# Optimization experiments

Hardware: AMD Instinct MI355X
Metric: run time of the kernel (lower is better)

Reference implementation:

```python
import jax, jax.numpy as jnp
import numpy as np

T, N, E, F, H, OUT = 6, 50000, 800000, 32, 64, 16


def _glorot(key, shape):
    lim = np.sqrt(6.0 / (shape[0] + shape[1])).astype(np.float32)
    return jax.random.uniform(key, shape, jnp.float32, -lim, lim)


def setup_inputs() -> dict:
    key = jax.random.key(0)
    ks = jax.random.split(key, 12)
    return {
        "xs": jax.random.normal(ks[0], (T, N, F), jnp.float32),
        "edge_index": jax.random.randint(ks[1], (T, 2, E), 0, N, jnp.int32),
        # GCNConv weights/biases for the z, r, h gates
        "Wz": _glorot(ks[2], (F, H)), "bz": jnp.zeros((H,), jnp.float32),
        "Wr": _glorot(ks[3], (F, H)), "br": jnp.zeros((H,), jnp.float32),
        "Wh": _glorot(ks[4], (F, H)), "bh": jnp.zeros((H,), jnp.float32),
        # Linear(2H -> H) per gate
        "Lz_W": _glorot(ks[5], (2 * H, H)), "Lz_b": jnp.zeros((H,), jnp.float32),
        "Lr_W": _glorot(ks[6], (2 * H, H)), "Lr_b": jnp.zeros((H,), jnp.float32),
        "Lh_W": _glorot(ks[7], (2 * H, H)), "Lh_b": jnp.zeros((H,), jnp.float32),
        # final Linear(H -> 16)
        "out_W": _glorot(ks[8], (H, OUT)), "out_b": jnp.zeros((OUT,), jnp.float32),
    }


def _gcn(x, W, b, src, dst):
    """GCNConv: D^-1/2 (A+I) D^-1/2 X W + b, edge list form."""
    n = x.shape[0]
    xw = x @ W  # [N,H] project first (cheaper than per-edge)
    loop = jnp.arange(n, dtype=src.dtype)
    s = jnp.concatenate([src, loop])
    d = jnp.concatenate([dst, loop])
    deg = jax.ops.segment_sum(jnp.ones_like(d, jnp.float32), d, num_segments=n)
    dinv = jnp.where(deg > 0, jax.lax.rsqrt(deg), 0.0)
    norm = dinv[s] * dinv[d]          # [E+N]
    msg = xw[s] * norm[:, None]       # gather + scale
    agg = jax.ops.segment_sum(msg, d, num_segments=n)  # scatter-add
    return agg + b


def reference(xs, edge_index, Wz, bz, Wr, br, Wh, bh,
              Lz_W, Lz_b, Lr_W, Lr_b, Lh_W, Lh_b, out_W, out_b):
    n = xs.shape[1]

    def step(h, inp):
        x, src, dst = inp
        Z = jax.nn.sigmoid(jnp.concatenate([_gcn(x, Wz, bz, src, dst), h], -1) @ Lz_W + Lz_b)
        R = jax.nn.sigmoid(jnp.concatenate([_gcn(x, Wr, br, src, dst), h], -1) @ Lr_W + Lr_b)
        Ht = jnp.tanh(jnp.concatenate([_gcn(x, Wh, bh, src, dst), h * R], -1) @ Lh_W + Lh_b)
        h_new = Z * h + (1.0 - Z) * Ht
        return h_new, None

    h0 = jnp.zeros((n, Wz.shape[1]), xs.dtype)
    h_final, _ = jax.lax.scan(step, h0, (xs, edge_index[:, 0], edge_index[:, 1]))
    return h_final @ out_W + out_b  # [N,16]
```

## Files before the change

### kernel.cpp

```cpp
#include <hip/hip_runtime.h>
#include <hip/hip_bf16.h>

#define TT 6
#define NN 50000
#define EE 800000
#define FF 32
#define HH 64
#define OO 16

#define NB 256
#define DPB 196
#define CHUNK 4096
#define CAP 4096

#define WFRAG_N 19456

typedef unsigned short ushort_t;
typedef unsigned char uchar_t;
typedef short short8 __attribute__((ext_vector_type(8)));
typedef float f32x4 __attribute__((ext_vector_type(4)));

__device__ __forceinline__ float ubf(ushort_t v){ return __uint_as_float(((unsigned)v) << 16); }
__device__ __forceinline__ ushort_t f2b(float f){
  unsigned u = __float_as_uint(f);
  return (ushort_t)((u + 0x7FFFu + ((u >> 16) & 1u)) >> 16);
}
__device__ __forceinline__ float lo16f(unsigned u){ return __uint_as_float(u << 16); }
__device__ __forceinline__ float hi16f(unsigned u){ return __uint_as_float(u & 0xFFFF0000u); }

__global__ void prepall_kernel(const float* __restrict__ Wz,const float* __restrict__ bz,
                               const float* __restrict__ Wr,const float* __restrict__ br,
                               const float* __restrict__ Wh,const float* __restrict__ bh,
                               const float* __restrict__ Lz,const float* __restrict__ Lzb,
                               const float* __restrict__ Lr,const float* __restrict__ Lrb,
                               const float* __restrict__ Lh,const float* __restrict__ Lhb,
                               const float* __restrict__ oW,const float* __restrict__ ob,
                               short* __restrict__ wfrag, float* __restrict__ wbias,
                               int* __restrict__ bcur){
  int bid = blockIdx.x, tid = threadIdx.x;
  if (bid < 76){
    int idx = bid*256 + tid;
    int slot = idx >> 9, lane = (idx >> 3) & 63, j = idx & 7;
    int q = lane >> 4, l15 = lane & 15;
    float val;
    if (slot < 36){
      int g, kc, ncol;
      if (slot < 24){ int nt = slot/3; kc = slot - nt*3; ncol = nt*16 + l15;
                      g = (ncol < 64) ? 0 : 1; ncol &= 63; }
      else          { int s2 = slot-24; int nt = s2/3; kc = s2 - nt*3;
                      ncol = nt*16 + l15; g = 2; }
      const float* W = (g==0)?Wz:((g==1)?Wr:Wh);
      const float* L = (g==0)?Lz:((g==1)?Lr:Lh);
      int k = kc*32 + q*8 + j;
      if (k < 32){
        float s = 0.f;
        for (int m = 0; m < 64; m++) s += W[k*64+m] * L[m*64+ncol];
        val = s;
      } else val = L[(32+k)*64 + ncol];
    } else {
      int kc = slot - 36;
      int k = kc*32 + q*8 + j;
      val = oW[k*16 + l15];
    }
    wfrag[idx] = (short)f2b(val);
  } else {
    if (tid < 192){
      int g = tid >> 6, j = tid & 63;
      const float* L  = (g==0)?Lz:((g==1)?Lr:Lh);
      const float* bb = (g==0)?bz:((g==1)?br:bh);
      const float* Lb = (g==0)?Lzb:((g==1)?Lrb:Lhb);
      float s = Lb[j];
      for (int m = 0; m < 64; m++) s += bb[m] * L[m*64+j];
      wbias[tid] = s;
    } else if (tid < 208){
      wbias[tid] = ob[tid-192];
    }
    for (int i = tid; i < 1536; i += 256) bcur[i] = 0;
  }
}

__global__ __launch_bounds__(256) void scatter_kernel(const int* __restrict__ ei,
                                                      int* __restrict__ bcur,
                                                      ushort_t* __restrict__ ssrc16,
                                                      uchar_t* __restrict__ sdst8){
  int t = blockIdx.y;
  __shared__ int cnt[NB];
  __shared__ int lstart[NB];
  __shared__ int gbase[NB];
  __shared__ int wsum[4];
  __shared__ ushort_t spay[CHUNK];
  __shared__ uchar_t  sdlo[CHUNK];
  __shared__ uchar_t  sbk[CHUNK];
  int tid = threadIdx.x;
  cnt[tid] = 0;
  __syncthreads();
  int e0 = blockIdx.x*CHUNK;
  const int* srcs = ei + t*2*EE;
  const int* dsts = ei + t*2*EE + EE;
  int pk[CHUNK/256];
  int ps[CHUNK/256];
  int pd[CHUNK/256];
  #pragma unroll
  for (int i = 0; i < CHUNK/256; i++){
    int e = e0 + i*256 + tid;
    if (e < EE){
      int s = srcs[e], d = dsts[e];
      int b = d / DPB;
      int lr = atomicAdd(&cnt[b], 1);
      pk[i] = (b << 12) | lr;
      ps[i] = s;
      pd[i] = d - b*DPB;
    } else pk[i] = -1;
  }
  __syncthreads();
  {
    int v = cnt[tid];
    int lane = tid & 63, wid = tid >> 6;
    int x = v;
    #pragma unroll
    for (int o = 1; o < 64; o <<= 1){
      int y = __shfl_up(x, o, 64);
      if (lane >= o) x += y;
    }
    if (lane == 63) wsum[wid] = x;
    __syncthreads();
    if (tid == 0){
      int s = 0;
      #pragma unroll
      for (int w = 0; w < 4; w++){ int tmp = wsum[w]; wsum[w] = s; s += tmp; }
    }
    __syncthreads();
    lstart[tid] = x - v + wsum[wid];
    gbase[tid] = (v > 0) ? atomicAdd(&bcur[t*NB + tid], v) : 0;
  }
  __syncthreads();
  #pragma unroll
  for (int i = 0; i < CHUNK/256; i++){
    if (pk[i] >= 0){
      int b = pk[i] >> 12, lr = pk[i] & 4095;
      int pos = lstart[b] + lr;
      spay[pos] = (ushort_t)ps[i];
      sdlo[pos] = (uchar_t)pd[i];
      sbk[pos]  = (uchar_t)b;
    }
  }
  __syncthreads();
  int nE = EE - e0; if (nE > CHUNK) nE = CHUNK;
  for (int i = tid; i < nE; i += 256){
    int b = sbk[i];
    int gpos = gbase[b] + (i - lstart[b]);
    if (gpos < CAP){
      size_t sb = (size_t)(t*NB + b)*CAP + gpos;
      ssrc16[sb] = spay[i];
      sdst8[sb]  = sdlo[i];
    }
  }
}

__global__ __launch_bounds__(256) void degdinv_kernel(const uchar_t* __restrict__ sdst8,
                                                      const int* __restrict__ bcur,
                                                      float* __restrict__ dinv){
  int b = blockIdx.x, t = blockIdx.y, tid = threadIdx.x;
  __shared__ int cnt[DPB];
  for (int i = tid; i < DPB; i += 256) cnt[i] = 0;
  __syncthreads();
  int ecnt = bcur[t*NB + b]; if (ecnt > CAP) ecnt = CAP;
  const uchar_t* dp = sdst8 + (size_t)(t*NB + b)*CAP;
  for (int i = tid; i < ecnt; i += 256)
    atomicAdd(&cnt[dp[i]], 1);
  __syncthreads();
  for (int i = tid; i < DPB; i += 256){
    int n = b*DPB + i;
    if (n < NN) dinv[t*NN + n] = rsqrtf((float)(cnt[i] + 1));
  }
}

__global__ void cvtscale_kernel(const float4* __restrict__ x4,
                                const float* __restrict__ dinv,
                                ushort4* __restrict__ xb4){
  int i = blockIdx.x*256 + threadIdx.x;
  if (i < TT*NN*8){
    float dn = dinv[i >> 3];
    float4 v = x4[i];
    ushort4 o;
    o.x = f2b(v.x*dn); o.y = f2b(v.y*dn); o.z = f2b(v.z*dn); o.w = f2b(v.w*dn);
    xb4[i] = o;
  }
}

__global__ __launch_bounds__(256) void gatherb_kernel(const ushort_t* __restrict__ xbs,
                                                      const ushort_t* __restrict__ ssrc16,
                                                      const uchar_t* __restrict__ sdst8,
                                                      const int* __restrict__ bcur,
                                                      ushort_t* __restrict__ aggb){
  int l = blockIdx.x;
  int wk = ((l & 7) * 192) + (l >> 3);
  int t = wk >> 8;
  int b = wk & 255;
  int tid = threadIdx.x;
  __shared__ ushort_t ssrc[CAP];
  __shared__ int scnt[DPB];
  __shared__ int soff[DPB + 1];
  __shared__ int scur[DPB];
  if (tid < DPB) scnt[tid] = 0;
  __syncthreads();
  int ecnt = bcur[t*NB + b]; if (ecnt > CAP) ecnt = CAP;
  size_t slab = (size_t)(t*NB + b)*CAP;
  const ushort_t* sp = ssrc16 + slab;
  const uchar_t*  dp = sdst8 + slab;
  for (int e = tid; e < ecnt; e += 256)
    atomicAdd(&scnt[dp[e]], 1);
  __syncthreads();
  if (tid < DPB) scur[tid] = scnt[tid];
  __syncthreads();
  for (int s = 1; s < DPB; s <<= 1){
    int v = 0;
    if (tid < DPB && tid >= s) v = scur[tid - s];
    __syncthreads();
    if (tid < DPB) scur[tid] += v;
    __syncthreads();
  }
  if (tid < DPB) soff[tid + 1] = scur[tid];
  if (tid == 0) soff[0] = 0;
  __syncthreads();
  if (tid < DPB) scur[tid] = soff[tid];
  __syncthreads();
  for (int e = tid; e < ecnt; e += 256){
    int ld = dp[e];
    int pos = atomicAdd(&scur[ld], 1);
    ssrc[pos] = sp[e];
  }
  __syncthreads();
  int wv = tid >> 6, lane = tid & 63;
  int g = lane >> 3, fp = lane & 7;
  const uint2* xb2 = (const uint2*)xbs + (size_t)t*NN*8;
  uint2* agg2 = (uint2*)aggb + (size_t)t*NN*8;
  for (int bb = wv; bb*8 < DPB; bb += 4){
    int ld = bb*8 + g;
    int e0 = 0, e1 = 0;
    if (ld < DPB){ e0 = soff[ld]; e1 = soff[ld + 1]; }
    float a0 = 0.f, a1 = 0.f, a2 = 0.f, a3 = 0.f;
    int i = e0;
    if (i < e1){
      int s = (int)ssrc[i];
      uint2 r = xb2[(size_t)s*8 + fp];
      for (++i; i < e1; ++i){
        int s2 = (int)ssrc[i];
        uint2 r2 = xb2[(size_t)s2*8 + fp];
        a0 += lo16f(r.x); a1 += hi16f(r.x);
        a2 += lo16f(r.y); a3 += hi16f(r.y);
        r = r2;
      }
      a0 += lo16f(r.x); a1 += hi16f(r.x);
      a2 += lo16f(r.y); a3 += hi16f(r.y);
    }
    int n = b*DPB + ld;
    if (ld < DPB && n < NN){
      float dn = rsqrtf((float)(e1 - e0 + 1));
      uint2 sv = xb2[(size_t)n*8 + fp];
      float o0 = dn*(a0 + lo16f(sv.x));
      float o1 = dn*(a1 + hi16f(sv.x));
      float o2 = dn*(a2 + lo16f(sv.y));
      float o3 = dn*(a3 + hi16f(sv.y));
      uint2 pk;
      pk.x = (unsigned)f2b(o0) | ((unsigned)f2b(o1) << 16);
      pk.y = (unsigned)f2b(o2) | ((unsigned)f2b(o3) << 16);
      agg2[(size_t)n*8 + fp] = pk;
    }
  }
}

__global__ __launch_bounds__(256) void gates_kernel(const ushort_t* __restrict__ aggb,
                                                    const float* __restrict__ wbias,
                                                    const short* __restrict__ wfrag,
                                                    float* __restrict__ out){
  __shared__ __align__(16) short Hsp[4096];
  __shared__ __align__(16) short HRp[4096];
  int tid = threadIdx.x;
  int nb = blockIdx.x*64;
  int wv = tid >> 6, lane = tid & 63;
  int q = lane >> 4, l15 = lane & 15;
  #pragma unroll
  for (int r = 0; r < 8; r++) ((int*)Hsp)[tid + 256*r] = 0;
  short8 wz[3], wr[3], wh[3];
  #pragma unroll
  for (int kc = 0; kc < 3; kc++){
    wz[kc] = ((const short8*)wfrag)[(wv*3 + kc)*64 + lane];
    wr[kc] = ((const short8*)wfrag)[((wv+4)*3 + kc)*64 + lane];
    wh[kc] = ((const short8*)wfrag)[(24 + wv*3 + kc)*64 + lane];
  }
  int jz = wv*16 + l15;
  float cz = wbias[jz], cr = wbias[64 + jz], ch = wbias[128 + jz];
  int c0 = jz >> 3, jl = jz & 7, x0 = c0 & 7;
  int sq0 = q & 7, sq1 = (4 + q) & 7;
  float hreg[4][4];
  #pragma unroll
  for (int mt = 0; mt < 4; mt++)
    #pragma unroll
    for (int e = 0; e < 4; e++) hreg[mt][e] = 0.f;
  f32x4 accZ[4], accH[4];
  const short8* agf = (const short8*)aggb;
  for (int t = 0; t < TT; t++){
    short8 fac[4];
    #pragma unroll
    for (int mt = 0; mt < 4; mt++){
      int gn = nb + mt*16 + l15;
      short8 v = {0,0,0,0,0,0,0,0};
      if (gn < NN) v = agf[((size_t)t*NN + gn)*4 + q];
      fac[mt] = v;
    }
    __syncthreads();
    #pragma unroll
    for (int mt = 0; mt < 4; mt++){
      int n = mt*16 + l15;
      short8 fh0 = *(const short8*)&Hsp[((q)*64   + (n ^ sq0))*8];
      short8 fh1 = *(const short8*)&Hsp[((4+q)*64 + (n ^ sq1))*8];
      f32x4 az = {0.f,0.f,0.f,0.f}, ar = {0.f,0.f,0.f,0.f};
      az = __builtin_amdgcn_mfma_f32_16x16x32_bf16(fac[mt], wz[0], az, 0,0,0);
      az = __builtin_amdgcn_mfma_f32_16x16x32_bf16(fh0,     wz[1], az, 0,0,0);
      az = __builtin_amdgcn_mfma_f32_16x16x32_bf16(fh1,     wz[2], az, 0,0,0);
      ar = __builtin_amdgcn_mfma_f32_16x16x32_bf16(fac[mt], wr[0], ar, 0,0,0);
      ar = __builtin_amdgcn_mfma_f32_16x16x32_bf16(fh0,     wr[1], ar, 0,0,0);
      ar = __builtin_amdgcn_mfma_f32_16x16x32_bf16(fh1,     wr[2], ar, 0,0,0);
      accZ[mt] = az; accH[mt] = ar;
    }
    #pragma unroll
    for (int mt = 0; mt < 4; mt++){
      #pragma unroll
      for (int e = 0; e < 4; e++){
        int node = mt*16 + q*4 + e;
        float z = __builtin_amdgcn_rcpf(1.f + __expf(-(accZ[mt][e] + cz)));
        float r = __builtin_amdgcn_rcpf(1.f + __expf(-(accH[mt][e] + cr)));
        HRp[(c0*64 + (node ^ x0))*8 + jl] = (short)f2b(hreg[mt][e] * r);
        accZ[mt][e] = z;
      }
    }
    __syncthreads();
    #pragma unroll
    for (int mt = 0; mt < 4; mt++){
      int n = mt*16 + l15;
      short8 fr0 = *(const short8*)&HRp[((q)*64   + (n ^ sq0))*8];
      short8 fr1 = *(const short8*)&HRp[((4+q)*64 + (n ^ sq1))*8];
      f32x4 ahh = {0.f,0.f,0.f,0.f};
      ahh = __builtin_amdgcn_mfma_f32_16x16x32_bf16(fac[mt], wh[0], ahh, 0,0,0);
      ahh = __builtin_amdgcn_mfma_f32_16x16x32_bf16(fr0,     wh[1], ahh, 0,0,0);
      ahh = __builtin_amdgcn_mfma_f32_16x16x32_bf16(fr1,     wh[2], ahh, 0,0,0);
      accH[mt] = ahh;
    }
    #pragma unroll
    for (int mt = 0; mt < 4; mt++){
      #pragma unroll
      for (int e = 0; e < 4; e++){
        int node = mt*16 + q*4 + e;
        float xv = accH[mt][e] + ch;
        float ex = __expf(-2.f*fabsf(xv));
        float th = (1.f - ex) * __builtin_amdgcn_rcpf(1.f + ex);
        th = (xv < 0.f) ? -th : th;
        float z = accZ[mt][e];
        float hv = z*hreg[mt][e] + (1.f - z)*th;
        hreg[mt][e] = hv;
        Hsp[(c0*64 + (node ^ x0))*8 + jl] = (short)f2b(hv);
      }
    }
  }
  __syncthreads();
  short8 wo0 = ((const short8*)wfrag)[36*64 + lane];
  short8 wo1 = ((const short8*)wfrag)[37*64 + lane];
  int no = wv*16 + l15;
  short8 f0 = *(const short8*)&Hsp[((q)*64   + (no ^ sq0))*8];
  short8 f1 = *(const short8*)&Hsp[((4+q)*64 + (no ^ sq1))*8];
  f32x4 ao = {0.f,0.f,0.f,0.f};
  ao = __builtin_amdgcn_mfma_f32_16x16x32_bf16(f0, wo0, ao, 0,0,0);
  ao = __builtin_amdgcn_mfma_f32_16x16x32_bf16(f1, wo1, ao, 0,0,0);
  float ob = wbias[192 + l15];
  #pragma unroll
  for (int e = 0; e < 4; e++){
    int gn = nb + wv*16 + q*4 + e;
    if (gn < NN) out[gn*OO + l15] = ao[e] + ob;
  }
}

extern "C" void kernel_launch(void* const* d_in, const int* in_sizes, int n_in,
                              void* d_out, int out_size, void* d_ws, size_t ws_size,
                              hipStream_t stream) {
  const float* xs = (const float*)d_in[0];
  const int*   ei = (const int*)d_in[1];
  float* out = (float*)d_out;
  char* ws = (char*)d_ws;
  ushort_t*  aggb   = (ushort_t*)(ws + 0);
  ushort_t*  xbs    = (ushort_t*)(ws + 19200000);
  ushort_t*  ssrc16 = (ushort_t*)(ws + 38400000);
  uchar_t*   sdst8  = (uchar_t*) (ws + 50982912);
  float*     dinv   = (float*)   (ws + 57274368);
  int*       bcur   = (int*)     (ws + 58474368);
  short*     wfrag  = (short*)   (ws + 58480512);
  float*     wbias  = (float*)   (ws + 58519424);

  prepall_kernel<<<77, 256, 0, stream>>>(
      (const float*)d_in[2],(const float*)d_in[3],(const float*)d_in[4],(const float*)d_in[5],
      (const float*)d_in[6],(const float*)d_in[7],(const float*)d_in[8],(const float*)d_in[9],
      (const float*)d_in[10],(const float*)d_in[11],(const float*)d_in[12],(const float*)d_in[13],
      (const float*)d_in[14],(const float*)d_in[15], wfrag, wbias, bcur);
  scatter_kernel<<<dim3((EE + CHUNK-1)/CHUNK, TT), 256, 0, stream>>>(ei, bcur, ssrc16, sdst8);
  degdinv_kernel<<<dim3(NB, TT), 256, 0, stream>>>(sdst8, bcur, dinv);
  cvtscale_kernel<<<(TT*NN*8 + 255)/256, 256, 0, stream>>>((const float4*)xs, dinv, (ushort4*)xbs);
  gatherb_kernel<<<NB*TT, 256, 0, stream>>>(xbs, ssrc16, sdst8, bcur, aggb);
  gates_kernel<<<(NN + 63)/64, 256, 0, stream>>>(aggb, wbias, wfrag, out);
}
```

Baseline: 261.9 us.

## Replace per-destination CSR sort in gather with LDS float atomic accumulation

The gather kernel no longer counts, prefix-sums and sorts edges by local destination in shared memory. Instead each group of four threads loads a source row as 16-byte chunks and atomically adds the eight bf16-decoded values into a padded fp32 shared-memory accumulator per destination. The kernel then scales by the precomputed dinv instead of recomputing it from the edge count. This removes the several barrier-heavy sort and scan phases and widens the global loads, at the cost of many LDS float atomics, possible contention on popular destinations, and a summation order that is no longer deterministic.

```diff
diff --git a/kernel.cpp b/kernel.cpp
--- a/kernel.cpp
+++ b/kernel.cpp
@@ -12,6 +12,7 @@
 #define DPB 196
 #define CHUNK 4096
 #define CAP 4096
+#define ASTR 33
 
 #define WFRAG_N 19456
 
@@ -192,80 +193,74 @@
                                                       const ushort_t* __restrict__ ssrc16,
                                                       const uchar_t* __restrict__ sdst8,
                                                       const int* __restrict__ bcur,
+                                                      const float* __restrict__ dinv,
                                                       ushort_t* __restrict__ aggb){
   int l = blockIdx.x;
   int wk = ((l & 7) * 192) + (l >> 3);
   int t = wk >> 8;
   int b = wk & 255;
   int tid = threadIdx.x;
-  __shared__ ushort_t ssrc[CAP];
-  __shared__ int scnt[DPB];
-  __shared__ int soff[DPB + 1];
-  __shared__ int scur[DPB];
-  if (tid < DPB) scnt[tid] = 0;
+  __shared__ float aggf[DPB*ASTR];
+  for (int i = tid; i < DPB*ASTR; i += 256) aggf[i] = 0.f;
   __syncthreads();
   int ecnt = bcur[t*NB + b]; if (ecnt > CAP) ecnt = CAP;
   size_t slab = (size_t)(t*NB + b)*CAP;
   const ushort_t* sp = ssrc16 + slab;
   const uchar_t*  dp = sdst8 + slab;
-  for (int e = tid; e < ecnt; e += 256)
-    atomicAdd(&scnt[dp[e]], 1);
-  __syncthreads();
-  if (tid < DPB) scur[tid] = scnt[tid];
-  __syncthreads();
-  for (int s = 1; s < DPB; s <<= 1){
-    int v = 0;
-    if (tid < DPB && tid >= s) v = scur[tid - s];
-    __syncthreads();
-    if (tid < DPB) scur[tid] += v;
-    __syncthreads();
-  }
-  if (tid < DPB) soff[tid + 1] = scur[tid];
-  if (tid == 0) soff[0] = 0;
-  __syncthreads();
-  if (tid < DPB) scur[tid] = soff[tid];
-  __syncthreads();
-  for (int e = tid; e < ecnt; e += 256){
-    int ld = dp[e];
-    int pos = atomicAdd(&scur[ld], 1);
-    ssrc[pos] = sp[e];
-  }
-  __syncthreads();
-  int wv = tid >> 6, lane = tid & 63;
-  int g = lane >> 3, fp = lane & 7;
-  const uint2* xb2 = (const uint2*)xbs + (size_t)t*NN*8;
-  uint2* agg2 = (uint2*)aggb + (size_t)t*NN*8;
-  for (int bb = wv; bb*8 < DPB; bb += 4){
-    int ld = bb*8 + g;
-    int e0 = 0, e1 = 0;
-    if (ld < DPB){ e0 = soff[ld]; e1 = soff[ld + 1]; }
-    float a0 = 0.f, a1 = 0.f, a2 = 0.f, a3 = 0.f;
-    int i = e0;
-    if (i < e1){
-      int s = (int)ssrc[i];
-      uint2 r = xb2[(size_t)s*8 + fp];
-      for (++i; i < e1; ++i){
-        int s2 = (int)ssrc[i];
-        uint2 r2 = xb2[(size_t)s2*8 + fp];
-        a0 += lo16f(r.x); a1 += hi16f(r.x);
-        a2 += lo16f(r.y); a3 += hi16f(r.y);
-        r = r2;
-      }
-      a0 += lo16f(r.x); a1 += hi16f(r.x);
-      a2 += lo16f(r.y); a3 += hi16f(r.y);
-    }
-    int n = b*DPB + ld;
-    if (ld < DPB && n < NN){
-      float dn = rsqrtf((float)(e1 - e0 + 1));
-      uint2 sv = xb2[(size_t)n*8 + fp];
-      float o0 = dn*(a0 + lo16f(sv.x));
-      float o1 = dn*(a1 + hi16f(sv.x));
-      float o2 = dn*(a2 + lo16f(sv.y));
-      float o3 = dn*(a3 + hi16f(sv.y));
-      uint2 pk;
+  const uint4* xb4 = (const uint4*)xbs + (size_t)t*NN*4;
+  int fp = tid & 3, eg = tid >> 2;
+  for (int e = eg; e < ecnt; e += 64*4){
+    int ss[4], dd[4]; bool vv[4];
+    #pragma unroll
+    for (int k = 0; k < 4; k++){
+      int ek = e + 64*k;
+      vv[k] = (ek < ecnt);
+      int idx = vv[k] ? ek : 0;
+      ss[k] = (int)sp[idx];
+      dd[k] = (int)dp[idx];
+    }
+    uint4 rr[4];
+    #pragma unroll
+    for (int k = 0; k < 4; k++)
+      rr[k] = xb4[(size_t)ss[k]*4 + fp];
+    #pragma unroll
+    for (int k = 0; k < 4; k++){
+      if (!vv[k]){ rr[k].x = 0u; rr[k].y = 0u; rr[k].z = 0u; rr[k].w = 0u; }
+      float* ap = &aggf[dd[k]*ASTR + fp*8];
+      atomicAdd(ap+0, lo16f(rr[k].x));
+      atomicAdd(ap+1, hi16f(rr[k].x));
+      atomicAdd(ap+2, lo16f(rr[k].y));
+      atomicAdd(ap+3, hi16f(rr[k].y));
+      atomicAdd(ap+4, lo16f(rr[k].z));
+      atomicAdd(ap+5, hi16f(rr[k].z));
+      atomicAdd(ap+6, lo16f(rr[k].w));
+      atomicAdd(ap+7, hi16f(rr[k].w));
+    }
+  }
+  __syncthreads();
+  const float* dv = dinv + (size_t)t*NN;
+  uint4* agg4 = (uint4*)aggb + (size_t)t*NN*4;
+  for (int i = tid; i < DPB*4; i += 256){
+    int d = i >> 2, fq = i & 3;
+    int n = b*DPB + d;
+    if (n < NN){
+      float dn = dv[n];
+      uint4 sv = xb4[(size_t)n*4 + fq];
+      const float* ap = &aggf[d*ASTR + fq*8];
+      float o0 = dn*(ap[0] + lo16f(sv.x));
+      float o1 = dn*(ap[1] + hi16f(sv.x));
+      float o2 = dn*(ap[2] + lo16f(sv.y));
+      float o3 = dn*(ap[3] + hi16f(sv.y));
+      float o4 = dn*(ap[4] + lo16f(sv.z));
+      float o5 = dn*(ap[5] + hi16f(sv.z));
+      float o6 = dn*(ap[6] + lo16f(sv.w));
+      float o7 = dn*(ap[7] + hi16f(sv.w));
+      uint4 pk;
       pk.x = (unsigned)f2b(o0) | ((unsigned)f2b(o1) << 16);
       pk.y = (unsigned)f2b(o2) | ((unsigned)f2b(o3) << 16);
-      agg2[(size_t)n*8 + fp] = pk;
+      pk.z = (unsigned)f2b(o4) | ((unsigned)f2b(o5) << 16);
+      pk.w = (unsigned)f2b(o6) | ((unsigned)f2b(o7) << 16);
+      agg4[(size_t)n*4 + fq] = pk;
     }
   }
 }
@@ -404,6 +399,6 @@
   scatter_kernel<<<dim3((EE + CHUNK-1)/CHUNK, TT), 256, 0, stream>>>(ei, bcur, ssrc16, sdst8);
   degdinv_kernel<<<dim3(NB, TT), 256, 0, stream>>>(sdst8, bcur, dinv);
   cvtscale_kernel<<<(TT*NN*8 + 255)/256, 256, 0, stream>>>((const float4*)xs, dinv, (ushort4*)xbs);
-  gatherb_kernel<<<NB*TT, 256, 0, stream>>>(xbs, ssrc16, sdst8, bcur, aggb);
+  gatherb_kernel<<<NB*TT, 256, 0, stream>>>(xbs, ssrc16, sdst8, bcur, dinv, aggb);
   gates_kernel<<<(NN + 63)/64, 256, 0, stream>>>(aggb, wbias, wfrag, out);
 }
```

New measurement: 998.7 us. +281.3%, slower.
